# Optimization experiments

Hardware: AMD Instinct MI355X
Metric: run time of the kernel (lower is better)

Reference implementation:

```python
import jax, jax.numpy as jnp
import numpy as np

N_NODES = 100000

def _graphconv_both(x, Wr, edges):
    # DGL GraphConv, norm='both', bias=False, allow_zero_in_degree=True:
    # out = D_in^{-1/2} * A^T_scatter( D_out^{-1/2}[src] * (X @ W)[src] )
    src, dst = edges[0], edges[1]
    ones = jnp.ones(src.shape[0], dtype=x.dtype)
    out_deg = jnp.clip(jax.ops.segment_sum(ones, src, num_segments=N_NODES), 1.0)
    in_deg = jnp.clip(jax.ops.segment_sum(ones, dst, num_segments=N_NODES), 1.0)
    norm_src = jax.lax.rsqrt(out_deg)  # [N]
    norm_dst = jax.lax.rsqrt(in_deg)   # [N]
    h = x @ Wr                          # [N, out] (mult W first since in>out)
    msg = h[src] * norm_src[src][:, None]          # [E, out]
    agg = jax.ops.segment_sum(msg, dst, num_segments=N_NODES)  # [N, out]
    return agg * norm_dst[:, None]


def setup_inputs() -> dict:
    key = jax.random.key(0)
    k1, k2, k3, k4 = jax.random.split(key, 4)
    x = jax.random.normal(k1, (N_NODES, 256), dtype=jnp.float32)
    W = jax.random.normal(k2, (4, 256, 64), dtype=jnp.float32) * 0.05
    src = jax.random.randint(k3, (4, 1, 1600000), 0, N_NODES)
    dst = jax.random.randint(k4, (4, 1, 1600000), 0, N_NODES)
    edge_index = jnp.concatenate([src, dst], axis=1).astype(jnp.int64)  # [4,2,E]
    return {"x": x, "W": W, "edge_index": edge_index}


def reference(x, W, edge_index):
    # per-relation GraphConv, stacked & summed, then tanh; dropout rate 0 -> identity
    per_rel = jax.vmap(lambda Wr, e: _graphconv_both(x, Wr, e))(W, edge_index)  # [R,N,out]
    Z = per_rel.sum(0)
    return jnp.tanh(Z)
```

## Files before the change

### kernel.cpp

```cpp
#include <hip/hip_runtime.h>
#include <hip/hip_bf16.h>

#define NN 100000
#define EPR 1600000
#define FIN 256
#define FOUT 64
#define BSZ 64
#define NB 1563
#define NBP 1568
#define CHUNK 4096
#define NBLK 391
#define EPT 16
#define CAP 4096
#define HSTRIDE ((size_t)(NN + 1) * FOUT)

typedef __attribute__((ext_vector_type(8))) short short8;
typedef __attribute__((ext_vector_type(4))) float f32x4;

__device__ __forceinline__ unsigned short f2bf(float f) {
    unsigned u = __float_as_uint(f);
    u = (u + 0x7FFFu + ((u >> 16) & 1u)) >> 16;
    return (unsigned short)u;
}
__device__ __forceinline__ float uaf(unsigned u) { return __uint_as_float(u); }
__device__ __forceinline__ void unpk(f32x4& seg, uint2 u) {
    seg.x += uaf(u.x << 16); seg.y += uaf(u.x & 0xFFFF0000u);
    seg.z += uaf(u.y << 16); seg.w += uaf(u.y & 0xFFFF0000u);
}

__global__ __launch_bounds__(256) void hist_all_kernel(const int* __restrict__ ei,
                                                       unsigned* __restrict__ btabD4,
                                                       unsigned* __restrict__ btabS4) {
    __shared__ unsigned hD[NB], hS[NB];
    int tid = threadIdx.x, r = blockIdx.y, blk = blockIdx.x;
    const int* src = ei + (size_t)r * 2 * EPR;
    const int* dst = src + EPR;
    for (int i = tid; i < NB; i += 256) { hD[i] = 0; hS[i] = 0; }
    __syncthreads();
    int e0 = blk * CHUNK;
    #pragma unroll
    for (int t = 0; t < EPT; ++t) {
        int e = e0 + t * 256 + tid;
        if (e < EPR) {
            atomicAdd(&hS[src[e] >> 6], 1u);
            atomicAdd(&hD[dst[e] >> 6], 1u);
        }
    }
    __syncthreads();
    size_t row = ((size_t)r * NBLK + blk) * NBP;
    for (int i = tid; i < NB; i += 256) {
        btabD4[row + i] = hD[i];
        btabS4[row + i] = hS[i];
    }
}

__global__ __launch_bounds__(256) void btot_all_kernel(unsigned* __restrict__ btabD4,
                                                       unsigned* __restrict__ btabS4,
                                                       unsigned* __restrict__ totD4,
                                                       unsigned* __restrict__ totS4) {
    int r = blockIdx.z;
    unsigned* tab = (blockIdx.y ? btabS4 : btabD4) + (size_t)r * NBLK * NBP;
    unsigned* tot = (blockIdx.y ? totS4 : totD4) + (size_t)r * NBP;
    __shared__ unsigned tile[NBLK][8];
    int b0 = blockIdx.x * 8;
    for (int idx = threadIdx.x; idx < NBLK * 8; idx += 256) {
        int blk = idx >> 3, bb = idx & 7;
        int b = b0 + bb;
        tile[blk][bb] = (b < NB) ? tab[(size_t)blk * NBP + b] : 0u;
    }
    __syncthreads();
    if (threadIdx.x < 8) {
        int bb = threadIdx.x;
        unsigned s = 0;
        for (int blk = 0; blk < NBLK; ++blk) {
            unsigned v = tile[blk][bb];
            tile[blk][bb] = s;
            s += v;
        }
        if (b0 + bb < NB) tot[b0 + bb] = s;
    }
    __syncthreads();
    for (int idx = threadIdx.x; idx < NBLK * 8; idx += 256) {
        int blk = idx >> 3, bb = idx & 7;
        int b = b0 + bb;
        if (b < NB) tab[(size_t)blk * NBP + b] = tile[blk][bb];
    }
}

__global__ void scan_all_kernel(const unsigned* __restrict__ totD4, const unsigned* __restrict__ totS4,
                                unsigned* __restrict__ gbaseD4, unsigned* __restrict__ gbaseS4) {
    int r = blockIdx.y;
    const unsigned* tot = (blockIdx.x ? totS4 : totD4) + (size_t)r * NBP;
    unsigned* gb = (blockIdx.x ? gbaseS4 : gbaseD4) + (size_t)r * NBP;
    __shared__ unsigned sc[256];
    int tid = threadIdx.x;
    unsigned loc[8]; unsigned s = 0;
    #pragma unroll
    for (int k = 0; k < 8; ++k) {
        int idx = tid * 8 + k;
        unsigned v = (idx < NB) ? tot[idx] : 0u;
        loc[k] = s; s += v;
    }
    sc[tid] = s; __syncthreads();
    for (int off = 1; off < 256; off <<= 1) {
        unsigned a = (tid >= off) ? sc[tid - off] : 0u;
        __syncthreads(); sc[tid] += a; __syncthreads();
    }
    unsigned texcl = tid ? sc[tid - 1] : 0u;
    #pragma unroll
    for (int k = 0; k < 8; ++k) {
        int idx = tid * 8 + k;
        if (idx < NB) gb[idx] = texcl + loc[k];
    }
}

__global__ __launch_bounds__(256) void place_all_kernel(const int* __restrict__ ei,
                                                        const unsigned* __restrict__ gbaseD4,
                                                        const unsigned* __restrict__ btabD4,
                                                        unsigned* __restrict__ pairs4,
                                                        const unsigned* __restrict__ gbaseS4,
                                                        const unsigned* __restrict__ btabS4,
                                                        unsigned char* __restrict__ pairs2_4) {
    __shared__ unsigned h[NB], hloc[NB], hbase[NB], sc[256];
    __shared__ unsigned buf[CHUNK], buf2[CHUNK];
    int tid = threadIdx.x, blk = blockIdx.x, r = blockIdx.y;
    const int* src = ei + (size_t)r * 2 * EPR;
    const int* dst = src + EPR;
    int e0 = blk * CHUNK;
    int csize = EPR - e0; if (csize > CHUNK) csize = CHUNK;

    int es[EPT], ed[EPT];
    #pragma unroll
    for (int t = 0; t < EPT; ++t) {
        int e = e0 + t * 256 + tid;
        if (e < EPR) { es[t] = src[e]; ed[t] = dst[e]; }
        else { es[t] = -1; ed[t] = 0; }
    }

    for (int i = tid; i < NB; i += 256) h[i] = 0;
    __syncthreads();
    #pragma unroll
    for (int t = 0; t < EPT; ++t)
        if (es[t] >= 0) atomicAdd(&h[ed[t] >> 6], 1u);
    __syncthreads();

    {
        unsigned loc[8]; unsigned s = 0;
        #pragma unroll
        for (int k = 0; k < 8; ++k) {
            int idx = tid * 8 + k;
            unsigned v = (idx < NB) ? h[idx] : 0u;
            loc[k] = s; s += v;
        }
        sc[tid] = s; __syncthreads();
        for (int off = 1; off < 256; off <<= 1) {
            unsigned a = (tid >= off) ? sc[tid - off] : 0u;
            __syncthreads(); sc[tid] += a; __syncthreads();
        }
        unsigned texcl = tid ? sc[tid - 1] : 0u;
        #pragma unroll
        for (int k = 0; k < 8; ++k) {
            int idx = tid * 8 + k;
            if (idx < NB) hloc[idx] = texcl + loc[k];
        }
    }
    __syncthreads();
    {
        const unsigned* gbase = gbaseD4 + (size_t)r * NBP;
        const unsigned* pblk = btabD4 + ((size_t)r * NBLK + blk) * NBP;
        for (int i = tid; i < NB; i += 256) hbase[i] = gbase[i] + pblk[i];
    }
    __syncthreads();
    for (int i = tid; i < NB; i += 256) h[i] = 0;
    __syncthreads();
    #pragma unroll
    for (int t = 0; t < EPT; ++t) {
        if (es[t] >= 0) {
            int b = ed[t] >> 6;
            unsigned rr = atomicAdd(&h[b], 1u);
            unsigned slot = hloc[b] + rr;
            buf[slot] = ((unsigned)es[t] << 7) | ((unsigned)(ed[t] & 63) << 24);
            buf2[slot] = hbase[b] + rr;
        }
    }
    __syncthreads();
    {
        unsigned* pairs = pairs4 + (size_t)r * EPR;
        for (int k = tid; k < csize; k += 256)
            pairs[buf2[k]] = buf[k];
    }
    __syncthreads();

    for (int i = tid; i < NB; i += 256) h[i] = 0;
    __syncthreads();
    #pragma unroll
    for (int t = 0; t < EPT; ++t)
        if (es[t] >= 0) atomicAdd(&h[es[t] >> 6], 1u);
    __syncthreads();

    {
        unsigned loc[8]; unsigned s = 0;
        #pragma unroll
        for (int k = 0; k < 8; ++k) {
            int idx = tid * 8 + k;
            unsigned v = (idx < NB) ? h[idx] : 0u;
            loc[k] = s; s += v;
        }
        sc[tid] = s; __syncthreads();
        for (int off = 1; off < 256; off <<= 1) {
            unsigned a = (tid >= off) ? sc[tid - off] : 0u;
            __syncthreads(); sc[tid] += a; __syncthreads();
        }
        unsigned texcl = tid ? sc[tid - 1] : 0u;
        #pragma unroll
        for (int k = 0; k < 8; ++k) {
            int idx = tid * 8 + k;
            if (idx < NB) hloc[idx] = texcl + loc[k];
        }
    }
    __syncthreads();
    {
        const unsigned* gbase = gbaseS4 + (size_t)r * NBP;
        const unsigned* pblk = btabS4 + ((size_t)r * NBLK + blk) * NBP;
        for (int i = tid; i < NB; i += 256) hbase[i] = gbase[i] + pblk[i];
    }
    __syncthreads();
    for (int i = tid; i < NB; i += 256) h[i] = 0;
    __syncthreads();
    {
        unsigned char* bufB = (unsigned char*)buf;
        #pragma unroll
        for (int t = 0; t < EPT; ++t) {
            if (es[t] >= 0) {
                int b = es[t] >> 6;
                unsigned rr = atomicAdd(&h[b], 1u);
                unsigned slot = hloc[b] + rr;
                bufB[slot] = (unsigned char)(es[t] & 63);
                buf2[slot] = hbase[b] + rr;
            }
        }
        __syncthreads();
        unsigned char* pairs2 = pairs2_4 + (size_t)r * EPR;
        for (int k = tid; k < csize; k += 256)
            pairs2[buf2[k]] = bufB[k];
    }
}

__global__ void srcdeg_all_kernel(const unsigned char* __restrict__ pairs2_4,
                                  const unsigned* __restrict__ gbaseS4,
                                  const unsigned* __restrict__ totS4,
                                  float* __restrict__ nsb4) {
    __shared__ unsigned cnt[BSZ];
    int tid = threadIdx.x, b = blockIdx.x, r = blockIdx.y;
    const unsigned char* pairs2 = pairs2_4 + (size_t)r * EPR;
    if (tid < BSZ) cnt[tid] = 0;
    __syncthreads();
    unsigned st = gbaseS4[(size_t)r * NBP + b];
    int n = (int)totS4[(size_t)r * NBP + b];
    for (int i = tid; i < n; i += 256)
        atomicAdd(&cnt[pairs2[st + i]], 1u);
    __syncthreads();
    if (tid < BSZ) {
        int node = b * BSZ + tid;
        if (node < NN) {
            unsigned c = cnt[tid]; if (c < 1u) c = 1u;
            nsb4[(size_t)r * NN + node] = rsqrtf((float)c);
        }
    }
}

__global__ __launch_bounds__(256, 2) void gemm4_kernel(const float* __restrict__ x,
                                                       const float* __restrict__ W,
                                                       unsigned short* __restrict__ hsb4,
                                                       const float* __restrict__ nsb4) {
    __shared__ unsigned short xs[128][40];
    __shared__ unsigned short wt[4][64][40];
    int tid = threadIdx.x;
    int wave = tid >> 6, lane = tid & 63;
    int wm = (wave >> 1) * 64;
    int wn = (wave & 1) * 32;
    int m0 = blockIdx.x * 128;

    f32x4 acc[4][4][2];
    #pragma unroll
    for (int r = 0; r < 4; ++r)
        #pragma unroll
        for (int mi = 0; mi < 4; ++mi)
            #pragma unroll
            for (int ni = 0; ni < 2; ++ni)
                acc[r][mi][ni] = (f32x4){0.f, 0.f, 0.f, 0.f};

    int srow = tid >> 1, skp = (tid & 1) * 16;
    int swn = tid >> 2, skq = (tid & 3) * 8;
    int gr = m0 + srow; if (gr >= NN) gr = NN - 1;
    const float* xrow = &x[(size_t)gr * FIN];

    for (int k0 = 0; k0 < FIN; k0 += 32) {
        #pragma unroll
        for (int q = 0; q < 4; ++q) {
            float4 v = *(const float4*)(xrow + k0 + skp + q * 4);
            unsigned lo = (unsigned)f2bf(v.x) | ((unsigned)f2bf(v.y) << 16);
            unsigned hi = (unsigned)f2bf(v.z) | ((unsigned)f2bf(v.w) << 16);
            *(uint2*)&xs[srow][skp + q * 4] = make_uint2(lo, hi);
        }
        #pragma unroll
        for (int r = 0; r < 4; ++r) {
            const float* w = W + (size_t)r * FIN * FOUT;
            unsigned pk[4];
            #pragma unroll
            for (int i = 0; i < 8; i += 2) {
                unsigned short b0 = f2bf(w[(size_t)(k0 + skq + i) * FOUT + swn]);
                unsigned short b1 = f2bf(w[(size_t)(k0 + skq + i + 1) * FOUT + swn]);
                pk[i >> 1] = (unsigned)b0 | ((unsigned)b1 << 16);
            }
            *(uint4*)&wt[r][swn][skq] = make_uint4(pk[0], pk[1], pk[2], pk[3]);
        }
        __syncthreads();

        int fr = lane & 15, fk = (lane >> 4) * 8;
        short8 af[4];
        #pragma unroll
        for (int mi = 0; mi < 4; ++mi) af[mi] = *(const short8*)&xs[wm + mi * 16 + fr][fk];
        #pragma unroll
        for (int r = 0; r < 4; ++r) {
            short8 b0 = *(const short8*)&wt[r][wn + fr][fk];
            short8 b1 = *(const short8*)&wt[r][wn + 16 + fr][fk];
            #pragma unroll
            for (int mi = 0; mi < 4; ++mi) {
                acc[r][mi][0] = __builtin_amdgcn_mfma_f32_16x16x32_bf16(af[mi], b0, acc[r][mi][0], 0, 0, 0);
                acc[r][mi][1] = __builtin_amdgcn_mfma_f32_16x16x32_bf16(af[mi], b1, acc[r][mi][1], 0, 0, 0);
            }
        }
        __syncthreads();
    }

    int fr = lane & 15, frow4 = (lane >> 4) * 4;
    #pragma unroll
    for (int r = 0; r < 4; ++r) {
        unsigned short* hsb = hsb4 + (size_t)r * HSTRIDE;
        const float* ns = nsb4 + (size_t)r * NN;
        #pragma unroll
        for (int mi = 0; mi < 4; ++mi) {
            #pragma unroll
            for (int rg = 0; rg < 4; ++rg) {
                int grow = m0 + wm + mi * 16 + frow4 + rg;
                if (grow < NN) {
                    float sc2 = ns[grow];
                    #pragma unroll
                    for (int ni = 0; ni < 2; ++ni) {
                        int gcol = wn + ni * 16 + fr;
                        hsb[(size_t)grow * FOUT + gcol] = f2bf(acc[r][mi][ni][rg] * sc2);
                    }
                }
            }
        }
    }
    if (blockIdx.x == 0 && tid < FOUT) {
        #pragma unroll
        for (int r = 0; r < 4; ++r)
            hsb4[(size_t)r * HSTRIDE + (size_t)NN * FOUT + tid] = 0;
    }
}

__global__ __launch_bounds__(512, 4) void aggsort4_kernel(const unsigned* __restrict__ pairs4,
                                                          const unsigned* __restrict__ gbaseD4,
                                                          const unsigned* __restrict__ totD4,
                                                          const unsigned short* __restrict__ hsb4,
                                                          float* __restrict__ out) {
    __shared__ unsigned sorted[CAP];
    __shared__ unsigned cnt[BSZ];
    __shared__ unsigned tdeg[BSZ];
    __shared__ unsigned loff[BSZ + 1];
    int tid = threadIdx.x;
    int b = blockIdx.x;
    int wave = tid >> 6, lane = tid & 63;
    int lg = lane >> 4;
    int lp = lane & 15;
    const unsigned DUMMY = (unsigned)NN << 7;

    f32x4 acc4[8];
    #pragma unroll
    for (int i = 0; i < 8; ++i) acc4[i] = (f32x4){0.f, 0.f, 0.f, 0.f};

    for (int r = 0; r < 4; ++r) {
        const unsigned* pairs = pairs4 + (size_t)r * EPR;
        const char* hsbB = (const char*)(hsb4 + (size_t)r * HSTRIDE) + (lp << 3);
        unsigned start = gbaseD4[(size_t)r * NBP + b];
        int n = (int)totD4[(size_t)r * NBP + b];

        __syncthreads();
        if (tid < BSZ) cnt[tid] = 0;
        __syncthreads();

        if (n <= CAP - 960) {
            unsigned rec[CAP / 512];
            #pragma unroll
            for (int t = 0; t < CAP / 512; ++t) {
                int i = t * 512 + tid;
                rec[t] = 0xFFFFFFFFu;
                if (i < n) {
                    rec[t] = pairs[start + i];
                    atomicAdd(&cnt[rec[t] >> 24], 1u);
                }
            }
            __syncthreads();
            if (wave == 0) {
                unsigned v = cnt[lane];
                unsigned pad = (v + 15u) & ~15u;
                unsigned sum = pad;
                #pragma unroll
                for (int o = 1; o < 64; o <<= 1) {
                    unsigned u = __shfl_up(sum, o);
                    if (lane >= o) sum += u;
                }
                loff[lane + 1] = sum;
                if (lane == 0) loff[0] = 0;
                tdeg[lane] = v;
                cnt[lane] = sum - pad;
            }
            __syncthreads();
            int ptot = (int)loff[BSZ];
            for (int i = tid; i < ptot; i += 512) sorted[i] = DUMMY;
            __syncthreads();
            #pragma unroll
            for (int t = 0; t < CAP / 512; ++t) {
                if (rec[t] != 0xFFFFFFFFu) {
                    unsigned p = atomicAdd(&cnt[rec[t] >> 24], 1u);
                    sorted[p] = rec[t];
                }
            }
            __syncthreads();

            #pragma unroll
            for (int i = 0; i < 8; ++i) {
                int nl = wave * 8 + i;
                int node = b * BSZ + nl;
                if (node >= NN) break;
                int lo = (int)loff[nl], hi = (int)loff[nl + 1];
                f32x4 seg = (f32x4){0.f, 0.f, 0.f, 0.f};
                for (int j0 = lo; j0 < hi; j0 += 16) {
                    unsigned q0 = sorted[j0 + lg];
                    unsigned q1 = sorted[j0 + 4 + lg];
                    unsigned q2 = sorted[j0 + 8 + lg];
                    unsigned q3 = sorted[j0 + 12 + lg];
                    uint2 u0 = *(const uint2*)(hsbB + (q0 & 0xFFFFFFu));
                    uint2 u1 = *(const uint2*)(hsbB + (q1 & 0xFFFFFFu));
                    uint2 u2 = *(const uint2*)(hsbB + (q2 & 0xFFFFFFu));
                    uint2 u3 = *(const uint2*)(hsbB + (q3 & 0xFFFFFFu));
                    unpk(seg, u0); unpk(seg, u1); unpk(seg, u2); unpk(seg, u3);
                }
                unsigned d = tdeg[nl]; if (d < 1u) d = 1u;
                float ndv = rsqrtf((float)d);
                acc4[i].x += seg.x * ndv;
                acc4[i].y += seg.y * ndv;
                acc4[i].z += seg.z * ndv;
                acc4[i].w += seg.w * ndv;
            }
        } else {
            for (int i = 0; i < 8; ++i) {
                int nl = wave * 8 + i;
                int node = b * BSZ + nl;
                if (node >= NN) break;
                f32x4 seg = (f32x4){0.f, 0.f, 0.f, 0.f};
                int deg = 0;
                for (int j = 0; j < n; ++j) {
                    unsigned q = pairs[start + j];
                    if ((int)(q >> 24) == nl) {
                        uint2 u = *(const uint2*)(hsbB + (q & 0xFFFFFFu));
                        unpk(seg, u);
                        ++deg;
                    }
                }
                if (deg < 1) deg = 1;
                float nv = rsqrtf((float)deg) * 0.25f;
                acc4[i].x += seg.x * nv; acc4[i].y += seg.y * nv;
                acc4[i].z += seg.z * nv; acc4[i].w += seg.w * nv;
            }
        }
    }

    #pragma unroll
    for (int i = 0; i < 8; ++i) {
        int nl = wave * 8 + i;
        int node = b * BSZ + nl;
        f32x4 v = acc4[i];
        v.x += __shfl_xor(v.x, 16); v.y += __shfl_xor(v.y, 16);
        v.z += __shfl_xor(v.z, 16); v.w += __shfl_xor(v.w, 16);
        v.x += __shfl_xor(v.x, 32); v.y += __shfl_xor(v.y, 32);
        v.z += __shfl_xor(v.z, 32); v.w += __shfl_xor(v.w, 32);
        if (node < NN && lg == 0) {
            float4 o;
            o.x = tanhf(v.x); o.y = tanhf(v.y); o.z = tanhf(v.z); o.w = tanhf(v.w);
            *(float4*)&out[(size_t)node * FOUT + lp * 4] = o;
        }
    }
}

extern "C" void kernel_launch(void* const* d_in, const int* in_sizes, int n_in,
                              void* d_out, int out_size, void* d_ws, size_t ws_size,
                              hipStream_t stream) {
    const float* x = (const float*)d_in[0];
    const float* W = (const float*)d_in[1];
    const int* ei = (const int*)d_in[2];
    float* out = (float*)d_out;

    char* ws = (char*)d_ws;
    size_t o = 0;
    unsigned short* hsb4 = (unsigned short*)(ws + o); o += (size_t)4 * HSTRIDE * 2;
    unsigned* pairs4 = (unsigned*)(ws + o);   o += (size_t)4 * EPR * 4;
    unsigned char* pairs2_4 = (unsigned char*)(ws + o); o += (size_t)4 * EPR;
    unsigned* btabD4 = (unsigned*)(ws + o);   o += (size_t)4 * NBLK * NBP * 4;
    unsigned* btabS4 = (unsigned*)(ws + o);   o += (size_t)4 * NBLK * NBP * 4;
    unsigned* totD4 = (unsigned*)(ws + o);    o += (size_t)4 * NBP * 4;
    unsigned* totS4 = (unsigned*)(ws + o);    o += (size_t)4 * NBP * 4;
    unsigned* gbaseD4 = (unsigned*)(ws + o);  o += (size_t)4 * NBP * 4;
    unsigned* gbaseS4 = (unsigned*)(ws + o);  o += (size_t)4 * NBP * 4;
    float* nsb4 = (float*)(ws + o);           o += (size_t)4 * NN * 4;

    hist_all_kernel<<<dim3(NBLK, 4), 256, 0, stream>>>(ei, btabD4, btabS4);
    btot_all_kernel<<<dim3((NB + 7) / 8, 2, 4), 256, 0, stream>>>(btabD4, btabS4, totD4, totS4);
    scan_all_kernel<<<dim3(2, 4), 256, 0, stream>>>(totD4, totS4, gbaseD4, gbaseS4);
    place_all_kernel<<<dim3(NBLK, 4), 256, 0, stream>>>(ei, gbaseD4, btabD4, pairs4,
                                                        gbaseS4, btabS4, pairs2_4);
    srcdeg_all_kernel<<<dim3(NB, 4), 256, 0, stream>>>(pairs2_4, gbaseS4, totS4, nsb4);
    gemm4_kernel<<<(NN + 127) / 128, 256, 0, stream>>>(x, W, hsb4, nsb4);
    aggsort4_kernel<<<NB, 512, 0, stream>>>(pairs4, gbaseD4, totD4, hsb4, out);
}
```

Baseline: 367.9 us.

## Halve destination bucket size to 32 nodes for finer aggregation blocks

Destination buckets shrink from 64 to 32 nodes, so the histogram, scan and placement stages use 3125 buckets and the aggregation kernel runs 3125 blocks of 256 threads with a smaller shared sort buffer. The placement kernel no longer precomputes a per-bucket global base table in shared memory. It packs the bucket and rank and looks up the global offsets at scatter time, which frees shared memory for the larger histogram. The aim is more parallelism and smaller LDS footprint in aggregation, at the cost of extra global lookups during scatter and more histogram or scan work.

```diff
diff --git a/kernel.cpp b/kernel.cpp
--- a/kernel.cpp
+++ b/kernel.cpp
@@ -8,10 +8,13 @@
 #define BSZ 64
 #define NB 1563
 #define NBP 1568
+#define BSZD 32
+#define NBD 3125
+#define NBPD 3136
 #define CHUNK 4096
 #define NBLK 391
 #define EPT 16
-#define CAP 4096
+#define CAP2 2048
 #define HSTRIDE ((size_t)(NN + 1) * FOUT)
 
 typedef __attribute__((ext_vector_type(8))) short short8;
@@ -31,11 +34,12 @@
 __global__ __launch_bounds__(256) void hist_all_kernel(const int* __restrict__ ei,
                                                        unsigned* __restrict__ btabD4,
                                                        unsigned* __restrict__ btabS4) {
-    __shared__ unsigned hD[NB], hS[NB];
+    __shared__ unsigned hD[NBD], hS[NB];
     int tid = threadIdx.x, r = blockIdx.y, blk = blockIdx.x;
     const int* src = ei + (size_t)r * 2 * EPR;
     const int* dst = src + EPR;
-    for (int i = tid; i < NB; i += 256) { hD[i] = 0; hS[i] = 0; }
+    for (int i = tid; i < NBD; i += 256) hD[i] = 0;
+    for (int i = tid; i < NB; i += 256) hS[i] = 0;
     __syncthreads();
     int e0 = blk * CHUNK;
     #pragma unroll
@@ -43,15 +47,14 @@
         int e = e0 + t * 256 + tid;
         if (e < EPR) {
             atomicAdd(&hS[src[e] >> 6], 1u);
-            atomicAdd(&hD[dst[e] >> 6], 1u);
-        }
-    }
-    __syncthreads();
-    size_t row = ((size_t)r * NBLK + blk) * NBP;
-    for (int i = tid; i < NB; i += 256) {
-        btabD4[row + i] = hD[i];
-        btabS4[row + i] = hS[i];
-    }
+            atomicAdd(&hD[dst[e] >> 5], 1u);
+        }
+    }
+    __syncthreads();
+    size_t rowD = ((size_t)r * NBLK + blk) * NBPD;
+    for (int i = tid; i < NBD; i += 256) btabD4[rowD + i] = hD[i];
+    size_t rowS = ((size_t)r * NBLK + blk) * NBP;
+    for (int i = tid; i < NB; i += 256) btabS4[rowS + i] = hS[i];
 }
 
 __global__ __launch_bounds__(256) void btot_all_kernel(unsigned* __restrict__ btabD4,
@@ -59,14 +62,17 @@
                                                        unsigned* __restrict__ totD4,
                                                        unsigned* __restrict__ totS4) {
     int r = blockIdx.z;
-    unsigned* tab = (blockIdx.y ? btabS4 : btabD4) + (size_t)r * NBLK * NBP;
-    unsigned* tot = (blockIdx.y ? totS4 : totD4) + (size_t)r * NBP;
+    int isS = blockIdx.y;
+    int NBcur = isS ? NB : NBD;
+    size_t NBPcur = isS ? NBP : NBPD;
+    unsigned* tab = (isS ? btabS4 : btabD4) + (size_t)r * NBLK * NBPcur;
+    unsigned* tot = (isS ? totS4 : totD4) + (size_t)r * NBPcur;
     __shared__ unsigned tile[NBLK][8];
     int b0 = blockIdx.x * 8;
     for (int idx = threadIdx.x; idx < NBLK * 8; idx += 256) {
         int blk = idx >> 3, bb = idx & 7;
         int b = b0 + bb;
-        tile[blk][bb] = (b < NB) ? tab[(size_t)blk * NBP + b] : 0u;
+        tile[blk][bb] = (b < NBcur) ? tab[(size_t)blk * NBPcur + b] : 0u;
     }
     __syncthreads();
     if (threadIdx.x < 8) {
@@ -77,28 +83,31 @@
             tile[blk][bb] = s;
             s += v;
         }
-        if (b0 + bb < NB) tot[b0 + bb] = s;
+        if (b0 + bb < NBcur) tot[b0 + bb] = s;
     }
     __syncthreads();
     for (int idx = threadIdx.x; idx < NBLK * 8; idx += 256) {
         int blk = idx >> 3, bb = idx & 7;
         int b = b0 + bb;
-        if (b < NB) tab[(size_t)blk * NBP + b] = tile[blk][bb];
+        if (b < NBcur) tab[(size_t)blk * NBPcur + b] = tile[blk][bb];
     }
 }
 
 __global__ void scan_all_kernel(const unsigned* __restrict__ totD4, const unsigned* __restrict__ totS4,
                                 unsigned* __restrict__ gbaseD4, unsigned* __restrict__ gbaseS4) {
     int r = blockIdx.y;
-    const unsigned* tot = (blockIdx.x ? totS4 : totD4) + (size_t)r * NBP;
-    unsigned* gb = (blockIdx.x ? gbaseS4 : gbaseD4) + (size_t)r * NBP;
+    int isS = blockIdx.x;
+    int NBcur = isS ? NB : NBD;
+    size_t NBPcur = isS ? NBP : NBPD;
+    const unsigned* tot = (isS ? totS4 : totD4) + (size_t)r * NBPcur;
+    unsigned* gb = (isS ? gbaseS4 : gbaseD4) + (size_t)r * NBPcur;
     __shared__ unsigned sc[256];
     int tid = threadIdx.x;
-    unsigned loc[8]; unsigned s = 0;
-    #pragma unroll
-    for (int k = 0; k < 8; ++k) {
-        int idx = tid * 8 + k;
-        unsigned v = (idx < NB) ? tot[idx] : 0u;
+    unsigned loc[16]; unsigned s = 0;
+    #pragma unroll
+    for (int k = 0; k < 16; ++k) {
+        int idx = tid * 16 + k;
+        unsigned v = (idx < NBcur) ? tot[idx] : 0u;
         loc[k] = s; s += v;
     }
     sc[tid] = s; __syncthreads();
@@ -108,9 +117,9 @@
     }
     unsigned texcl = tid ? sc[tid - 1] : 0u;
     #pragma unroll
-    for (int k = 0; k < 8; ++k) {
-        int idx = tid * 8 + k;
-        if (idx < NB) gb[idx] = texcl + loc[k];
+    for (int k = 0; k < 16; ++k) {
+        int idx = tid * 16 + k;
+        if (idx < NBcur) gb[idx] = texcl + loc[k];
     }
 }
 
@@ -121,7 +130,7 @@
                                                         const unsigned* __restrict__ gbaseS4,
                                                         const unsigned* __restrict__ btabS4,
                                                         unsigned char* __restrict__ pairs2_4) {
-    __shared__ unsigned h[NB], hloc[NB], hbase[NB], sc[256];
+    __shared__ unsigned h[NBD], hloc[NBD], sc[256];
     __shared__ unsigned buf[CHUNK], buf2[CHUNK];
     int tid = threadIdx.x, blk = blockIdx.x, r = blockIdx.y;
     const int* src = ei + (size_t)r * 2 * EPR;
@@ -137,19 +146,18 @@
         else { es[t] = -1; ed[t] = 0; }
     }
 
-    for (int i = tid; i < NB; i += 256) h[i] = 0;
+    for (int i = tid; i < NBD; i += 256) h[i] = 0;
     __syncthreads();
     #pragma unroll
     for (int t = 0; t < EPT; ++t)
-        if (es[t] >= 0) atomicAdd(&h[ed[t] >> 6], 1u);
-    __syncthreads();
-
+        if (es[t] >= 0) atomicAdd(&h[ed[t] >> 5], 1u);
+    __syncthreads();
     {
-        unsigned loc[8]; unsigned s = 0;
-        #pragma unroll
-        for (int k = 0; k < 8; ++k) {
-            int idx = tid * 8 + k;
-            unsigned v = (idx < NB) ? h[idx] : 0u;
+        unsigned loc[16]; unsigned s = 0;
+        #pragma unroll
+        for (int k = 0; k < 16; ++k) {
+            int idx = tid * 16 + k;
+            unsigned v = (idx < NBD) ? h[idx] : 0u;
             loc[k] = s; s += v;
         }
         sc[tid] = s; __syncthreads();
@@ -159,35 +167,34 @@
         }
         unsigned texcl = tid ? sc[tid - 1] : 0u;
         #pragma unroll
-        for (int k = 0; k < 8; ++k) {
-            int idx = tid * 8 + k;
-            if (idx < NB) hloc[idx] = texcl + loc[k];
-        }
-    }
-    __syncthreads();
-    {
-        const unsigned* gbase = gbaseD4 + (size_t)r * NBP;
-        const unsigned* pblk = btabD4 + ((size_t)r * NBLK + blk) * NBP;
-        for (int i = tid; i < NB; i += 256) hbase[i] = gbase[i] + pblk[i];
-    }
-    __syncthreads();
-    for (int i = tid; i < NB; i += 256) h[i] = 0;
+        for (int k = 0; k < 16; ++k) {
+            int idx = tid * 16 + k;
+            if (idx < NBD) hloc[idx] = texcl + loc[k];
+        }
+    }
+    __syncthreads();
+    for (int i = tid; i < NBD; i += 256) h[i] = 0;
     __syncthreads();
     #pragma unroll
     for (int t = 0; t < EPT; ++t) {
         if (es[t] >= 0) {
-            int b = ed[t] >> 6;
-            unsigned rr = atomicAdd(&h[b], 1u);
-            unsigned slot = hloc[b] + rr;
-            buf[slot] = ((unsigned)es[t] << 7) | ((unsigned)(ed[t] & 63) << 24);
-            buf2[slot] = hbase[b] + rr;
+            int b = ed[t] >> 5;
+            unsigned rk = atomicAdd(&h[b], 1u);
+            unsigned slot = hloc[b] + rk;
+            buf[slot] = ((unsigned)es[t] << 7) | ((unsigned)(ed[t] & 31) << 24);
+            buf2[slot] = ((unsigned)b << 13) | rk;
         }
     }
     __syncthreads();
     {
         unsigned* pairs = pairs4 + (size_t)r * EPR;
-        for (int k = tid; k < csize; k += 256)
-            pairs[buf2[k]] = buf[k];
+        const unsigned* gb = gbaseD4 + (size_t)r * NBPD;
+        const unsigned* pb = btabD4 + ((size_t)r * NBLK + blk) * NBPD;
+        for (int k = tid; k < csize; k += 256) {
+            unsigned u = buf2[k];
+            unsigned bb = u >> 13, rk = u & 8191u;
+            pairs[gb[bb] + pb[bb] + rk] = buf[k];
+        }
     }
     __syncthreads();
 
@@ -197,12 +204,11 @@
     for (int t = 0; t < EPT; ++t)
         if (es[t] >= 0) atomicAdd(&h[es[t] >> 6], 1u);
     __syncthreads();
-
     {
-        unsigned loc[8]; unsigned s = 0;
-        #pragma unroll
-        for (int k = 0; k < 8; ++k) {
-            int idx = tid * 8 + k;
+        unsigned loc[16]; unsigned s = 0;
+        #pragma unroll
+        for (int k = 0; k < 16; ++k) {
+            int idx = tid * 16 + k;
             unsigned v = (idx < NB) ? h[idx] : 0u;
             loc[k] = s; s += v;
         }
@@ -213,16 +219,10 @@
         }
         unsigned texcl = tid ? sc[tid - 1] : 0u;
         #pragma unroll
-        for (int k = 0; k < 8; ++k) {
-            int idx = tid * 8 + k;
+        for (int k = 0; k < 16; ++k) {
+            int idx = tid * 16 + k;
             if (idx < NB) hloc[idx] = texcl + loc[k];
         }
-    }
-    __syncthreads();
-    {
-        const unsigned* gbase = gbaseS4 + (size_t)r * NBP;
-        const unsigned* pblk = btabS4 + ((size_t)r * NBLK + blk) * NBP;
-        for (int i = tid; i < NB; i += 256) hbase[i] = gbase[i] + pblk[i];
     }
     __syncthreads();
     for (int i = tid; i < NB; i += 256) h[i] = 0;
@@ -233,16 +233,21 @@
         for (int t = 0; t < EPT; ++t) {
             if (es[t] >= 0) {
                 int b = es[t] >> 6;
-                unsigned rr = atomicAdd(&h[b], 1u);
-                unsigned slot = hloc[b] + rr;
+                unsigned rk = atomicAdd(&h[b], 1u);
+                unsigned slot = hloc[b] + rk;
                 bufB[slot] = (unsigned char)(es[t] & 63);
-                buf2[slot] = hbase[b] + rr;
+                buf2[slot] = ((unsigned)b << 13) | rk;
             }
         }
         __syncthreads();
         unsigned char* pairs2 = pairs2_4 + (size_t)r * EPR;
-        for (int k = tid; k < csize; k += 256)
-            pairs2[buf2[k]] = bufB[k];
+        const unsigned* gb = gbaseS4 + (size_t)r * NBP;
+        const unsigned* pb = btabS4 + ((size_t)r * NBLK + blk) * NBP;
+        for (int k = tid; k < csize; k += 256) {
+            unsigned u = buf2[k];
+            unsigned bb = u >> 13, rk = u & 8191u;
+            pairs2[gb[bb] + pb[bb] + rk] = bufB[k];
+        }
     }
 }
 
@@ -362,15 +367,15 @@
     }
 }
 
-__global__ __launch_bounds__(512, 4) void aggsort4_kernel(const unsigned* __restrict__ pairs4,
+__global__ __launch_bounds__(256, 4) void aggsort4_kernel(const unsigned* __restrict__ pairs4,
                                                           const unsigned* __restrict__ gbaseD4,
                                                           const unsigned* __restrict__ totD4,
                                                           const unsigned short* __restrict__ hsb4,
                                                           float* __restrict__ out) {
-    __shared__ unsigned sorted[CAP];
-    __shared__ unsigned cnt[BSZ];
-    __shared__ unsigned tdeg[BSZ];
-    __shared__ unsigned loff[BSZ + 1];
+    __shared__ unsigned sorted[CAP2];
+    __shared__ unsigned cnt[BSZD];
+    __shared__ unsigned tdeg[BSZD];
+    __shared__ unsigned loff[BSZD + 1];
     int tid = threadIdx.x;
     int b = blockIdx.x;
     int wave = tid >> 6, lane = tid & 63;
@@ -385,18 +390,18 @@
     for (int r = 0; r < 4; ++r) {
         const unsigned* pairs = pairs4 + (size_t)r * EPR;
         const char* hsbB = (const char*)(hsb4 + (size_t)r * HSTRIDE) + (lp << 3);
-        unsigned start = gbaseD4[(size_t)r * NBP + b];
-        int n = (int)totD4[(size_t)r * NBP + b];
+        unsigned start = gbaseD4[(size_t)r * NBPD + b];
+        int n = (int)totD4[(size_t)r * NBPD + b];
 
         __syncthreads();
-        if (tid < BSZ) cnt[tid] = 0;
+        if (tid < BSZD) cnt[tid] = 0;
         __syncthreads();
 
-        if (n <= CAP - 960) {
-            unsigned rec[CAP / 512];
-            #pragma unroll
-            for (int t = 0; t < CAP / 512; ++t) {
-                int i = t * 512 + tid;
+        if (n <= CAP2 - 480) {
+            unsigned rec[CAP2 / 256];
+            #pragma unroll
+            for (int t = 0; t < CAP2 / 256; ++t) {
+                int i = t * 256 + tid;
                 rec[t] = 0xFFFFFFFFu;
                 if (i < n) {
                     rec[t] = pairs[start + i];
@@ -405,7 +410,7 @@
             }
             __syncthreads();
             if (wave == 0) {
-                unsigned v = cnt[lane];
+                unsigned v = (lane < BSZD) ? cnt[lane] : 0u;
                 unsigned pad = (v + 15u) & ~15u;
                 unsigned sum = pad;
                 #pragma unroll
@@ -413,17 +418,19 @@
                     unsigned u = __shfl_up(sum, o);
                     if (lane >= o) sum += u;
                 }
-                loff[lane + 1] = sum;
+                if (lane < BSZD) {
+                    loff[lane + 1] = sum;
+                    tdeg[lane] = v;
+                    cnt[lane] = sum - pad;
+                }
                 if (lane == 0) loff[0] = 0;
-                tdeg[lane] = v;
-                cnt[lane] = sum - pad;
             }
             __syncthreads();
-            int ptot = (int)loff[BSZ];
-            for (int i = tid; i < ptot; i += 512) sorted[i] = DUMMY;
+            int ptot = (int)loff[BSZD];
+            for (int i = tid; i < ptot; i += 256) sorted[i] = DUMMY;
             __syncthreads();
             #pragma unroll
-            for (int t = 0; t < CAP / 512; ++t) {
+            for (int t = 0; t < CAP2 / 256; ++t) {
                 if (rec[t] != 0xFFFFFFFFu) {
                     unsigned p = atomicAdd(&cnt[rec[t] >> 24], 1u);
                     sorted[p] = rec[t];
@@ -434,8 +441,6 @@
             #pragma unroll
             for (int i = 0; i < 8; ++i) {
                 int nl = wave * 8 + i;
-                int node = b * BSZ + nl;
-                if (node >= NN) break;
                 int lo = (int)loff[nl], hi = (int)loff[nl + 1];
                 f32x4 seg = (f32x4){0.f, 0.f, 0.f, 0.f};
                 for (int j0 = lo; j0 < hi; j0 += 16) {
@@ -459,8 +464,6 @@
         } else {
             for (int i = 0; i < 8; ++i) {
                 int nl = wave * 8 + i;
-                int node = b * BSZ + nl;
-                if (node >= NN) break;
                 f32x4 seg = (f32x4){0.f, 0.f, 0.f, 0.f};
                 int deg = 0;
                 for (int j = 0; j < n; ++j) {
@@ -482,13 +485,13 @@
     #pragma unroll
     for (int i = 0; i < 8; ++i) {
         int nl = wave * 8 + i;
-        int node = b * BSZ + nl;
+        int node = b * BSZD + nl;
         f32x4 v = acc4[i];
         v.x += __shfl_xor(v.x, 16); v.y += __shfl_xor(v.y, 16);
         v.z += __shfl_xor(v.z, 16); v.w += __shfl_xor(v.w, 16);
         v.x += __shfl_xor(v.x, 32); v.y += __shfl_xor(v.y, 32);
         v.z += __shfl_xor(v.z, 32); v.w += __shfl_xor(v.w, 32);
-        if (node < NN && lg == 0) {
+        if (lg == 0) {
             float4 o;
             o.x = tanhf(v.x); o.y = tanhf(v.y); o.z = tanhf(v.z); o.w = tanhf(v.w);
             *(float4*)&out[(size_t)node * FOUT + lp * 4] = o;
@@ -509,20 +512,20 @@
     unsigned short* hsb4 = (unsigned short*)(ws + o); o += (size_t)4 * HSTRIDE * 2;
     unsigned* pairs4 = (unsigned*)(ws + o);   o += (size_t)4 * EPR * 4;
     unsigned char* pairs2_4 = (unsigned char*)(ws + o); o += (size_t)4 * EPR;
-    unsigned* btabD4 = (unsigned*)(ws + o);   o += (size_t)4 * NBLK * NBP * 4;
+    unsigned* btabD4 = (unsigned*)(ws + o);   o += (size_t)4 * NBLK * NBPD * 4;
     unsigned* btabS4 = (unsigned*)(ws + o);   o += (size_t)4 * NBLK * NBP * 4;
-    unsigned* totD4 = (unsigned*)(ws + o);    o += (size_t)4 * NBP * 4;
+    unsigned* totD4 = (unsigned*)(ws + o);    o += (size_t)4 * NBPD * 4;
     unsigned* totS4 = (unsigned*)(ws + o);    o += (size_t)4 * NBP * 4;
-    unsigned* gbaseD4 = (unsigned*)(ws + o);  o += (size_t)4 * NBP * 4;
+    unsigned* gbaseD4 = (unsigned*)(ws + o);  o += (size_t)4 * NBPD * 4;
     unsigned* gbaseS4 = (unsigned*)(ws + o);  o += (size_t)4 * NBP * 4;
     float* nsb4 = (float*)(ws + o);           o += (size_t)4 * NN * 4;
 
     hist_all_kernel<<<dim3(NBLK, 4), 256, 0, stream>>>(ei, btabD4, btabS4);
-    btot_all_kernel<<<dim3((NB + 7) / 8, 2, 4), 256, 0, stream>>>(btabD4, btabS4, totD4, totS4);
+    btot_all_kernel<<<dim3(NBPD / 8, 2, 4), 256, 0, stream>>>(btabD4, btabS4, totD4, totS4);
     scan_all_kernel<<<dim3(2, 4), 256, 0, stream>>>(totD4, totS4, gbaseD4, gbaseS4);
     place_all_kernel<<<dim3(NBLK, 4), 256, 0, stream>>>(ei, gbaseD4, btabD4, pairs4,
                                                         gbaseS4, btabS4, pairs2_4);
     srcdeg_all_kernel<<<dim3(NB, 4), 256, 0, stream>>>(pairs2_4, gbaseS4, totS4, nsb4);
     gemm4_kernel<<<(NN + 127) / 128, 256, 0, stream>>>(x, W, hsb4, nsb4);
-    aggsort4_kernel<<<NB, 512, 0, stream>>>(pairs4, gbaseD4, totD4, hsb4, out);
-}
+    aggsort4_kernel<<<NBD, 256, 0, stream>>>(pairs4, gbaseD4, totD4, hsb4, out);
+}
```

Result: slower. 393.9 us (+7.1%).
